# Kernel optimization log

Measured on AMD Instinct MI355X. Metric: run time of the kernel, lower is better.

Reference implementation:

```python
import jax, jax.numpy as jnp
import numpy as np

B, S = 4096, 4096
NS, FDIM = 16, 64


def _ln(x, g, b):
    mu = jnp.mean(x, axis=-1, keepdims=True)
    v = jnp.mean((x - mu) ** 2, axis=-1, keepdims=True)
    return (x - mu) / jnp.sqrt(v + 1e-5) * g + b


def _rolling_vol_mean(returns, w):
    # mean over all length-w windows of unbiased std (matches per-window torch.std loop)
    Bn, L = returns.shape
    z = jnp.zeros((Bn, 1), returns.dtype)
    c1 = jnp.concatenate([z, jnp.cumsum(returns, axis=1)], axis=1)
    c2 = jnp.concatenate([z, jnp.cumsum(returns * returns, axis=1)], axis=1)
    s = c1[:, w:] - c1[:, :-w]    # [B, L-w+1] window sums
    s2 = c2[:, w:] - c2[:, :-w]
    var = (s2 - s * s / w) / (w - 1)
    return jnp.mean(jnp.sqrt(jnp.maximum(var, 0.0)), axis=1, keepdims=True)


def setup_inputs() -> dict:
    key = jax.random.key(0)
    ks = jax.random.split(key, 24)
    r = lambda i, shp: jax.random.normal(ks[i], shp, jnp.float32) * 0.05
    return {
        'price_series': jax.random.uniform(ks[0], (B, S, 1), jnp.float32) * 10.0 + 1.0,
        're_W': r(1, (4, 4, 64)), 're_b': r(2, (4, 64)),
        're_g': jnp.ones((4, 64), jnp.float32), 're_beta': jnp.zeros((4, 64), jnp.float32),
        'rh_W1': r(3, (256, 64)), 'rh_b1': r(4, (64,)), 'rh_W2': r(5, (64, 4)), 'rh_b2': r(6, (4,)),
        'rv_W': r(7, (3, 128)), 'rv_b': r(8, (128,)),
        'rv_g': jnp.ones((128,), jnp.float32), 'rv_beta': jnp.zeros((128,), jnp.float32),
        'vs_W': r(9, (128, 128)), 'vs_b': r(10, (128,)),
        'vs_g': jnp.ones((128,), jnp.float32), 'vs_beta': jnp.zeros((128,), jnp.float32),
        'vc_W1': r(11, (256, 64)), 'vc_b1': r(12, (64,)), 'vc_W2': r(13, (64, 4)), 'vc_b2': r(14, (4,)),
        'emb': r(15, (NS, FDIM)),
        'cn_W1': r(16, (576, 128)), 'cn_b1': r(17, (128,)),
        'cn_W2': r(18, (128, 64)), 'cn_b2': r(19, (64,)),
        'cn_W3': r(20, (64, 1)), 'cn_b3': r(21, (1,)),
    }


def reference(price_series, re_W, re_b, re_g, re_beta, rh_W1, rh_b1, rh_W2, rh_b2,
              rv_W, rv_b, rv_g, rv_beta, vs_W, vs_b, vs_g, vs_beta,
              vc_W1, vc_b1, vc_W2, vc_b2, emb, cn_W1, cn_b1, cn_W2, cn_b2, cn_W3, cn_b3):
    prices = price_series[:, :, 0]            # [B,S]
    Bn, Sn = prices.shape
    # --- MarketRegimeEncoder: SMA-20 via prefix sums (the per-step torch loop) ---
    cs = jnp.cumsum(prices, axis=1)
    shifted = jnp.concatenate([jnp.zeros((Bn, 20), prices.dtype), cs[:, :-20]], axis=1)
    counts = jnp.minimum(jnp.arange(Sn) + 1, 20).astype(prices.dtype)
    sma20 = (cs - shifted) / counts           # (sma_5 is computed but unused in original)
    trend = jnp.mean((prices - sma20) / (sma20 + 1e-8), axis=1, keepdims=True)
    p10 = prices[:, Sn - 10:Sn - 9]
    momentum = (prices[:, -1:] - p10) / (p10 + 1e-8)
    pmean = jnp.mean(prices, axis=1, keepdims=True)
    mean_rev = (prices[:, -1:] - pmean) / (pmean + 1e-8)
    pstd = jnp.std(prices, axis=1, keepdims=True, ddof=1)
    cycle = pstd / (pmean + 1e-8)
    combined = jnp.concatenate([trend, momentum, mean_rev, cycle], axis=1)  # [B,4]
    h = jax.nn.relu(jnp.einsum('bi,kio->bko', combined, re_W) + re_b[None])  # [B,4,64]
    h = _ln(h, re_g[None], re_beta[None])
    regime_features = h.reshape(Bn, -1)        # [B,256] (trend|momentum|mean_rev|cycle)
    logits = jax.nn.relu(regime_features @ rh_W1 + rh_b1) @ rh_W2 + rh_b2
    regime_probs = jax.nn.softmax(logits, axis=1)
    # --- VolatilityEncodingModule ---
    logp = jnp.log(jnp.maximum(price_series, 1e-8))
    returns = jnp.diff(logp, axis=1)[:, :, 0]  # [B,S-1]
    vol_in = jnp.concatenate([_rolling_vol_mean(returns, w) for w in (5, 10, 20)], axis=1)  # [B,3]
    rv = _ln(jax.nn.relu(vol_in @ rv_W + rv_b), rv_g, rv_beta)
    vs = _ln(jax.nn.relu(rv @ vs_W + vs_b), vs_g, vs_beta)
    vol_features = jnp.concatenate([rv, vs], axis=1)  # [B,256]
    vlogits = jax.nn.relu(vol_features @ vc_W1 + vc_b1) @ vc_W2 + vc_b2
    vol_regime = jax.nn.softmax(vlogits, axis=1)
    # --- OptionsStrategyEncoder: vectorized over strategies ---
    mv = jnp.concatenate([regime_features, vol_features], axis=1)  # [B,512]
    mvp = mv @ cn_W1[:512]                    # [B,128]
    ep = emb @ cn_W1[512:]                    # [NS,128]
    h1 = jax.nn.relu(mvp[:, None, :] + ep[None, :, :] + cn_b1)  # [B,NS,128]
    h2 = jax.nn.relu(h1 @ cn_W2 + cn_b2)      # [B,NS,64]
    scores = (h2 @ cn_W3 + cn_b3)[:, :, 0]    # [B,NS]
    return regime_features, regime_probs, vol_features, vol_regime, scores
```

## Files before the change

kernel.cpp:

```cpp
#include <hip/hip_runtime.h>
#include <math.h>

#define NROWS 4096
#define SLEN  4096
#define RETN  4095
#define CHK   20

__global__ __launch_bounds__(256) void k_ep(const float* __restrict__ emb,
                                            const float* __restrict__ cn_W1,
                                            const float* __restrict__ cn_b1,
                                            float* __restrict__ ep) {
    int idx = blockIdx.x * 256 + threadIdx.x;
    if (idx >= 16 * 128) return;
    int n = idx >> 7, o = idx & 127;
    float acc = cn_b1[o];
    const float* w = cn_W1 + 512 * 128;
    for (int i = 0; i < 64; ++i) acc = fmaf(emb[n * 64 + i], w[i * 128 + o], acc);
    ep[idx] = acc;
}

__global__ void k_stats(const float* __restrict__ price,
                        float* __restrict__ combined,
                        float* __restrict__ volin) {
    __shared__ float scm[260 * CHK];
    __shared__ float red[6][4];

    const int tid = threadIdx.x;
    const int row = blockIdx.x;
    const float* pr = price + (size_t)row * SLEN;

    float pA = 0.f, pB = 0.f;
    if (tid == 0) { pA = pr[SLEN - 10]; pB = pr[SLEN - 1]; }

    if (tid < 40) { scm[tid] = 0.f; scm[258 * CHK + tid] = 0.f; }

    #pragma unroll
    for (int it = 0; it < 4; ++it) {
        const int i = it * 256 + tid;
        const float4 v = ((const float4*)pr)[i];
        *(float4*)&scm[(2 + (i >> 2)) * CHK + ((4 * i) & 15)] = v;
    }
    __syncthreads();

    const int s0 = tid * 16;

    float hb[20], x_[16];
    *(float4*)&hb[0] = *(const float4*)&scm[tid * CHK + 12];
    #pragma unroll
    for (int k = 0; k < 4; ++k)
        *(float4*)&hb[4 + 4 * k] = *(const float4*)&scm[(tid + 1) * CHK + 4 * k];
    #pragma unroll
    for (int k = 0; k < 4; ++k)
        *(float4*)&x_[4 * k] = *(const float4*)&scm[(tid + 2) * CHK + 4 * k];
    const float pn = scm[(tid + 3) * CHK];

    float W = 0.f;
    #pragma unroll
    for (int k = 0; k < 20; ++k) W += hb[k];
    float st = 0.f, s1p = 0.f, s2p = 0.f;
    #pragma unroll
    for (int d = 0; d < 16; ++d) {
        const float x = x_[d];
        W += x - hb[d];
        float inv_cnt = 0.05f;
        if (s0 == 0)                 inv_cnt = 1.0f / (float)(d + 1);
        else if (s0 == 16 && d < 3)  inv_cnt = 1.0f / (float)(17 + d);
        const float sma = W * inv_cnt;
        st  = fmaf(x - sma, __builtin_amdgcn_rcpf(sma + 1e-8f), st);
        s1p += x;
        s2p = fmaf(x, x, s2p);
    }

    float lg[17];
    #pragma unroll
    for (int d = 0; d < 16; ++d) lg[d] = __builtin_amdgcn_logf(fmaxf(x_[d], 1e-8f));
    lg[16] = __builtin_amdgcn_logf(fmaxf(pn, 1e-8f));
    float rs[36];
    #pragma unroll
    for (int d = 0; d < 16; ++d) rs[d] = lg[d + 1] - lg[d];

    __syncthreads();
    #pragma unroll
    for (int k = 0; k < 4; ++k)
        *(float4*)&scm[(tid + 2) * CHK + 4 * k] = *(const float4*)&rs[4 * k];
    __syncthreads();

    #pragma unroll
    for (int k = 0; k < 4; ++k)
        *(float4*)&rs[16 + 4 * k] = *(const float4*)&scm[(tid + 3) * CHK + 4 * k];
    *(float4*)&rs[32] = *(const float4*)&scm[(tid + 4) * CHK];

    float S5 = 0.f, Q5 = 0.f, S10 = 0.f, Q10 = 0.f, S20 = 0.f, Q20 = 0.f;
    #pragma unroll
    for (int j = 0; j < 20; ++j) {
        const float x = rs[j];
        S20 += x; Q20 = fmaf(x, x, Q20);
        if (j < 10) { S10 += x; Q10 = fmaf(x, x, Q10); }
        if (j < 5)  { S5  += x; Q5  = fmaf(x, x, Q5); }
    }

    #define SQT(S, Q, invw) \
        __builtin_amdgcn_sqrtf(fmaxf(fmaf(-(S) * (invw), (S), (Q)), 0.f))

    float v5 = 0.f, v10 = 0.f, v20 = 0.f;
    if (tid < 254) {
        #pragma unroll
        for (int d = 0; d < 16; ++d) {
            v5  += SQT(S5,  Q5,  0.2f);
            v10 += SQT(S10, Q10, 0.1f);
            v20 += SQT(S20, Q20, 0.05f);
            const float xo = rs[d], qo = xo * xo;
            const float a5 = rs[d + 5], a10 = rs[d + 10], a20 = rs[d + 20];
            S5  += a5  - xo;  Q5  = fmaf(a5,  a5,  Q5)  - qo;
            S10 += a10 - xo;  Q10 = fmaf(a10, a10, Q10) - qo;
            S20 += a20 - xo;  Q20 = fmaf(a20, a20, Q20) - qo;
        }
    } else {
        #pragma unroll
        for (int d = 0; d < 16; ++d) {
            const int i = s0 + d;
            if (i < 4091) v5  += SQT(S5,  Q5,  0.2f);
            if (i < 4086) v10 += SQT(S10, Q10, 0.1f);
            if (i < 4076) v20 += SQT(S20, Q20, 0.05f);
            const float xo = rs[d], qo = xo * xo;
            const float a5 = rs[d + 5], a10 = rs[d + 10], a20 = rs[d + 20];
            S5  += a5  - xo;  Q5  = fmaf(a5,  a5,  Q5)  - qo;
            S10 += a10 - xo;  Q10 = fmaf(a10, a10, Q10) - qo;
            S20 += a20 - xo;  Q20 = fmaf(a20, a20, Q20) - qo;
        }
    }
    #undef SQT

    {
        float vals[6] = {s1p, s2p, st, v5, v10, v20};
        const int lane = tid & 63, wid = tid >> 6;
        #pragma unroll
        for (int v = 0; v < 6; ++v) {
            float x = vals[v];
            for (int o = 32; o > 0; o >>= 1) x += __shfl_xor(x, o, 64);
            if (lane == 0) red[v][wid] = x;
        }
    }
    __syncthreads();
    if (tid == 0) {
        const float sum_p  = red[0][0] + red[0][1] + red[0][2] + red[0][3];
        const float sum_p2 = red[1][0] + red[1][1] + red[1][2] + red[1][3];
        const float sum_t  = red[2][0] + red[2][1] + red[2][2] + red[2][3];
        const float sv5    = red[3][0] + red[3][1] + red[3][2] + red[3][3];
        const float sv10   = red[4][0] + red[4][1] + red[4][2] + red[4][3];
        const float sv20   = red[5][0] + red[5][1] + red[5][2] + red[5][3];
        const float pmean = sum_p * (1.f / 4096.f);
        const float varp  = fmaf(-sum_p * (1.f / 4096.f), sum_p, sum_p2) * (1.f / 4095.f);
        const float pstd  = __builtin_amdgcn_sqrtf(fmaxf(varp, 0.f));
        const float ipm   = __builtin_amdgcn_rcpf(pmean + 1e-8f);
        combined[row * 4 + 0] = sum_t * (1.f / 4096.f);
        combined[row * 4 + 1] = (pB - pA) * __builtin_amdgcn_rcpf(pA + 1e-8f);
        combined[row * 4 + 2] = (pB - pmean) * ipm;
        combined[row * 4 + 3] = pstd * ipm;
        const float LN2 = 0.6931471805599453f;
        volin[row * 3 + 0] = sv5  * (LN2 * 0.5f                 / 4091.f);
        volin[row * 3 + 1] = sv10 * (LN2 * (1.f / 3.f)          / 4086.f);
        volin[row * 3 + 2] = sv20 * (LN2 * 0.22941573387056174f / 4076.f);
    }
}

__global__ __launch_bounds__(256) void k_mc(const float* __restrict__ combined,
                                            const float* __restrict__ volin,
                                            const float* __restrict__ re_W,  const float* __restrict__ re_b,
                                            const float* __restrict__ re_g,  const float* __restrict__ re_be,
                                            const float* __restrict__ rh_W1, const float* __restrict__ rh_b1,
                                            const float* __restrict__ rh_W2, const float* __restrict__ rh_b2,
                                            const float* __restrict__ rv_W,  const float* __restrict__ rv_b,
                                            const float* __restrict__ rv_g,  const float* __restrict__ rv_be,
                                            const float* __restrict__ vs_W,  const float* __restrict__ vs_b,
                                            const float* __restrict__ vs_g,  const float* __restrict__ vs_be,
                                            const float* __restrict__ vc_W1, const float* __restrict__ vc_b1,
                                            const float* __restrict__ vc_W2, const float* __restrict__ vc_b2,
                                            const float* __restrict__ cn_W1,
                                            const float* __restrict__ cn_W2,
                                            const float* __restrict__ cn_b2,
                                            const float* __restrict__ cn_W3,
                                            const float* __restrict__ cn_b3,
                                            const float* __restrict__ ep,
                                            float* __restrict__ out_rf, float* __restrict__ out_rp,
                                            float* __restrict__ out_vf, float* __restrict__ out_vr,
                                            float* __restrict__ scores) {
    __shared__ __align__(16) float w2s[128 * 64];
    __shared__ __align__(16) float epb[16][132];
    __shared__ __align__(16) float rf_lds[8][256];
    __shared__ __align__(16) float vf_lds[8][256];
    __shared__ __align__(16) float psx[4][8][128];
    __shared__ __align__(16) float mvp_s[8][132];
    __shared__ float hid_s[8][64];
    __shared__ float prt[4][8];
    __shared__ float cmb_s[8][4];
    __shared__ float vol_s[8][3];

    const int tid  = threadIdx.x;
    const int lane = tid & 63;
    const int wid  = tid >> 6;
    const int row0 = blockIdx.x * 8;

    #pragma unroll
    for (int k = 0; k < 8; ++k) {
        const int idx = k * 256 + tid;
        *(float4*)&w2s[4 * idx] = *(const float4*)(cn_W2 + 4 * idx);
    }
    {
        const int ns = tid >> 4, c8 = (tid & 15) * 8;
        *(float4*)&epb[ns][c8]     = *(const float4*)(ep + ns * 128 + c8);
        *(float4*)&epb[ns][c8 + 4] = *(const float4*)(ep + ns * 128 + c8 + 4);
    }
    if (tid < 32) cmb_s[tid >> 2][tid & 3] = combined[(size_t)(row0 + (tid >> 2)) * 4 + (tid & 3)];
    else if (tid < 56) { int t = tid - 32; vol_s[t / 3][t % 3] = volin[(size_t)(row0 + t / 3) * 3 + t % 3]; }
    __syncthreads();

    {
        const float* w = re_W + wid * 256;
        const float w0 = w[lane], w1 = w[64 + lane], w2 = w[128 + lane], w3 = w[192 + lane];
        const float b  = re_b[wid * 64 + lane];
        const float gg = re_g[wid * 64 + lane], bb = re_be[wid * 64 + lane];
        float h[8], sm[8], sq[8];
        #pragma unroll
        for (int r = 0; r < 8; ++r) {
            float v = fmaf(cmb_s[r][0], w0, fmaf(cmb_s[r][1], w1,
                      fmaf(cmb_s[r][2], w2, fmaf(cmb_s[r][3], w3, b))));
            h[r] = fmaxf(v, 0.f);
            sm[r] = h[r]; sq[r] = h[r] * h[r];
        }
        #pragma unroll
        for (int off = 32; off > 0; off >>= 1) {
            #pragma unroll
            for (int r = 0; r < 8; ++r) {
                sm[r] += __shfl_xor(sm[r], off, 64);
                sq[r] += __shfl_xor(sq[r], off, 64);
            }
        }
        #pragma unroll
        for (int r = 0; r < 8; ++r) {
            const float mu  = sm[r] * (1.f / 64.f);
            const float var = fmaxf(sq[r] * (1.f / 64.f) - mu * mu, 0.f);
            const float y = (h[r] - mu) * rsqrtf(var + 1e-5f) * gg + bb;
            rf_lds[r][wid * 64 + lane] = y;
            out_rf[(size_t)(row0 + r) * 256 + wid * 64 + lane] = y;
        }
    }
    __syncthreads();

    {
        const int i0 = wid * 64;
        float acc[8] = {0.f, 0.f, 0.f, 0.f, 0.f, 0.f, 0.f, 0.f};
        for (int i = 0; i < 64; ++i) {
            const float wv = rh_W1[(size_t)(i0 + i) * 64 + lane];
            #pragma unroll
            for (int r = 0; r < 8; ++r) acc[r] = fmaf(rf_lds[r][i0 + i], wv, acc[r]);
        }
        #pragma unroll
        for (int r = 0; r < 8; ++r) psx[wid][r][lane] = acc[r];
    }
    __syncthreads();

    for (int it = tid; it < 512; it += 256) {
        const int r = it >> 6, o = it & 63;
        const float v = psx[0][r][o] + psx[1][r][o] + psx[2][r][o] + psx[3][r][o] + rh_b1[o];
        hid_s[r][o] = fmaxf(v, 0.f);
    }
    __syncthreads();

    if (tid < 32) {
        const int r = tid >> 2, j = tid & 3;
        float acc = rh_b2[j];
        for (int i = 0; i < 64; ++i) acc = fmaf(hid_s[r][i], rh_W2[i * 4 + j], acc);
        float m = acc;
        m = fmaxf(m, __shfl_xor(m, 1, 64));
        m = fmaxf(m, __shfl_xor(m, 2, 64));
        const float e = expf(acc - m);
        float s = e;
        s += __shfl_xor(s, 1, 64);
        s += __shfl_xor(s, 2, 64);
        out_rp[(size_t)(row0 + r) * 4 + j] = e / s;
    }

    {
        const int o = tid & 127, g = tid >> 7, wv_ = tid >> 6;
        const float w0 = rv_W[o], w1 = rv_W[128 + o], w2 = rv_W[256 + o];
        const float b = rv_b[o], gg = rv_g[o], bb = rv_be[o];
        float h[4], sm[4], sq[4];
        #pragma unroll
        for (int r4 = 0; r4 < 4; ++r4) {
            const int r = g * 4 + r4;
            float v = fmaf(vol_s[r][0], w0, fmaf(vol_s[r][1], w1, fmaf(vol_s[r][2], w2, b)));
            h[r4] = fmaxf(v, 0.f);
            sm[r4] = h[r4]; sq[r4] = h[r4] * h[r4];
        }
        #pragma unroll
        for (int off = 32; off > 0; off >>= 1) {
            #pragma unroll
            for (int r4 = 0; r4 < 4; ++r4) {
                sm[r4] += __shfl_xor(sm[r4], off, 64);
                sq[r4] += __shfl_xor(sq[r4], off, 64);
            }
        }
        if (lane == 0) {
            #pragma unroll
            for (int r4 = 0; r4 < 4; ++r4) { prt[wv_][r4 * 2] = sm[r4]; prt[wv_][r4 * 2 + 1] = sq[r4]; }
        }
        __syncthreads();
        #pragma unroll
        for (int r4 = 0; r4 < 4; ++r4) {
            const float S = prt[2 * g][2 * r4]     + prt[2 * g + 1][2 * r4];
            const float Q = prt[2 * g][2 * r4 + 1] + prt[2 * g + 1][2 * r4 + 1];
            const float mu  = S * (1.f / 128.f);
            const float var = fmaxf(Q * (1.f / 128.f) - mu * mu, 0.f);
            const float y = (h[r4] - mu) * rsqrtf(var + 1e-5f) * gg + bb;
            vf_lds[g * 4 + r4][o] = y;
            out_vf[(size_t)(row0 + g * 4 + r4) * 256 + o] = y;
        }
    }
    __syncthreads();

    {
        const int o = tid & 127, g = tid >> 7, wv_ = tid >> 6;
        float acc[4];
        const float b = vs_b[o];
        #pragma unroll
        for (int r4 = 0; r4 < 4; ++r4) acc[r4] = b;
        for (int i = 0; i < 128; ++i) {
            const float wv = vs_W[(size_t)i * 128 + o];
            #pragma unroll
            for (int r4 = 0; r4 < 4; ++r4) acc[r4] = fmaf(vf_lds[g * 4 + r4][i], wv, acc[r4]);
        }
        const float gg = vs_g[o], bb = vs_be[o];
        float h[4], sm[4], sq[4];
        #pragma unroll
        for (int r4 = 0; r4 < 4; ++r4) {
            h[r4] = fmaxf(acc[r4], 0.f);
            sm[r4] = h[r4]; sq[r4] = h[r4] * h[r4];
        }
        #pragma unroll
        for (int off = 32; off > 0; off >>= 1) {
            #pragma unroll
            for (int r4 = 0; r4 < 4; ++r4) {
                sm[r4] += __shfl_xor(sm[r4], off, 64);
                sq[r4] += __shfl_xor(sq[r4], off, 64);
            }
        }
        __syncthreads();
        if (lane == 0) {
            #pragma unroll
            for (int r4 = 0; r4 < 4; ++r4) { prt[wv_][r4 * 2] = sm[r4]; prt[wv_][r4 * 2 + 1] = sq[r4]; }
        }
        __syncthreads();
        #pragma unroll
        for (int r4 = 0; r4 < 4; ++r4) {
            const float S = prt[2 * g][2 * r4]     + prt[2 * g + 1][2 * r4];
            const float Q = prt[2 * g][2 * r4 + 1] + prt[2 * g + 1][2 * r4 + 1];
            const float mu  = S * (1.f / 128.f);
            const float var = fmaxf(Q * (1.f / 128.f) - mu * mu, 0.f);
            const float y = (h[r4] - mu) * rsqrtf(var + 1e-5f) * gg + bb;
            vf_lds[g * 4 + r4][128 + o] = y;
            out_vf[(size_t)(row0 + g * 4 + r4) * 256 + 128 + o] = y;
        }
    }
    __syncthreads();

    {
        const int i0 = wid * 64;
        float acc[8] = {0.f, 0.f, 0.f, 0.f, 0.f, 0.f, 0.f, 0.f};
        for (int i = 0; i < 64; ++i) {
            const float wv = vc_W1[(size_t)(i0 + i) * 64 + lane];
            #pragma unroll
            for (int r = 0; r < 8; ++r) acc[r] = fmaf(vf_lds[r][i0 + i], wv, acc[r]);
        }
        #pragma unroll
        for (int r = 0; r < 8; ++r) psx[wid][r][lane] = acc[r];
    }
    __syncthreads();

    for (int it = tid; it < 512; it += 256) {
        const int r = it >> 6, o = it & 63;
        const float v = psx[0][r][o] + psx[1][r][o] + psx[2][r][o] + psx[3][r][o] + vc_b1[o];
        hid_s[r][o] = fmaxf(v, 0.f);
    }
    __syncthreads();
    if (tid < 32) {
        const int r = tid >> 2, j = tid & 3;
        float acc = vc_b2[j];
        for (int i = 0; i < 64; ++i) acc = fmaf(hid_s[r][i], vc_W2[i * 4 + j], acc);
        float m = acc;
        m = fmaxf(m, __shfl_xor(m, 1, 64));
        m = fmaxf(m, __shfl_xor(m, 2, 64));
        const float e = expf(acc - m);
        float s = e;
        s += __shfl_xor(s, 1, 64);
        s += __shfl_xor(s, 2, 64);
        out_vr[(size_t)(row0 + r) * 4 + j] = e / s;
    }
    __syncthreads();

    {
        const int p = lane >> 5;
        const int q = lane & 31;
        const float* mbase = (wid < 2) ? &rf_lds[0][0] + wid * 128
                                       : &vf_lds[0][0] + (wid - 2) * 128;
        float acc[8][4] = {{0.f}};
        #pragma unroll 8
        for (int s = 0; s < 64; ++s) {
            const int i = 2 * s + p;
            const float4 w1v = *(const float4*)(cn_W1 + (size_t)(wid * 128 + i) * 128 + 4 * q);
            #pragma unroll
            for (int r = 0; r < 8; ++r) {
                const float m = mbase[r * 256 + i];
                acc[r][0] = fmaf(m, w1v.x, acc[r][0]);
                acc[r][1] = fmaf(m, w1v.y, acc[r][1]);
                acc[r][2] = fmaf(m, w1v.z, acc[r][2]);
                acc[r][3] = fmaf(m, w1v.w, acc[r][3]);
            }
        }
        #pragma unroll
        for (int r = 0; r < 8; ++r) {
            #pragma unroll
            for (int k = 0; k < 4; ++k) acc[r][k] += __shfl_xor(acc[r][k], 32, 64);
        }
        if (p == 0) {
            #pragma unroll
            for (int r = 0; r < 8; ++r)
                *(float4*)&psx[wid][r][4 * q] =
                    make_float4(acc[r][0], acc[r][1], acc[r][2], acc[r][3]);
        }
    }
    __syncthreads();

    #pragma unroll
    for (int k = 0; k < 4; ++k) {
        const int idx = k * 256 + tid;
        const int r = idx >> 7, c = idx & 127;
        mvp_s[r][c] = psx[0][r][c] + psx[1][r][c] + psx[2][r][c] + psx[3][r][c];
    }
    __syncthreads();

    {
        const int ns = tid >> 4;
        const int t  = tid & 15;
        float acc[8][4];
        #pragma unroll
        for (int r = 0; r < 8; ++r)
            #pragma unroll
            for (int k = 0; k < 4; ++k) acc[r][k] = 0.f;

        #pragma unroll 2
        for (int c = 0; c < 128; c += 4) {
            float4 m4[8];
            #pragma unroll
            for (int r = 0; r < 8; ++r) m4[r] = *(const float4*)&mvp_s[r][c];
            const float4 e4 = *(const float4*)&epb[ns][c];
            {   const float4 w2v = *(const float4*)&w2s[(c + 0) * 64 + 4 * t];
                #pragma unroll
                for (int r = 0; r < 8; ++r) {
                    const float h = fmaxf(m4[r].x + e4.x, 0.f);
                    acc[r][0] = fmaf(h, w2v.x, acc[r][0]); acc[r][1] = fmaf(h, w2v.y, acc[r][1]);
                    acc[r][2] = fmaf(h, w2v.z, acc[r][2]); acc[r][3] = fmaf(h, w2v.w, acc[r][3]); } }
            {   const float4 w2v = *(const float4*)&w2s[(c + 1) * 64 + 4 * t];
                #pragma unroll
                for (int r = 0; r < 8; ++r) {
                    const float h = fmaxf(m4[r].y + e4.y, 0.f);
                    acc[r][0] = fmaf(h, w2v.x, acc[r][0]); acc[r][1] = fmaf(h, w2v.y, acc[r][1]);
                    acc[r][2] = fmaf(h, w2v.z, acc[r][2]); acc[r][3] = fmaf(h, w2v.w, acc[r][3]); } }
            {   const float4 w2v = *(const float4*)&w2s[(c + 2) * 64 + 4 * t];
                #pragma unroll
                for (int r = 0; r < 8; ++r) {
                    const float h = fmaxf(m4[r].z + e4.z, 0.f);
                    acc[r][0] = fmaf(h, w2v.x, acc[r][0]); acc[r][1] = fmaf(h, w2v.y, acc[r][1]);
                    acc[r][2] = fmaf(h, w2v.z, acc[r][2]); acc[r][3] = fmaf(h, w2v.w, acc[r][3]); } }
            {   const float4 w2v = *(const float4*)&w2s[(c + 3) * 64 + 4 * t];
                #pragma unroll
                for (int r = 0; r < 8; ++r) {
                    const float h = fmaxf(m4[r].w + e4.w, 0.f);
                    acc[r][0] = fmaf(h, w2v.x, acc[r][0]); acc[r][1] = fmaf(h, w2v.y, acc[r][1]);
                    acc[r][2] = fmaf(h, w2v.z, acc[r][2]); acc[r][3] = fmaf(h, w2v.w, acc[r][3]); } }
        }

        const float4 b2v = *(const float4*)(cn_b2 + 4 * t);
        const float4 w3v = *(const float4*)(cn_W3 + 4 * t);
        const float  b3v = cn_b3[0];
        #pragma unroll
        for (int r = 0; r < 8; ++r) {
            float s =      fmaxf(acc[r][0] + b2v.x, 0.f) * w3v.x;
            s = fmaf(fmaxf(acc[r][1] + b2v.y, 0.f), w3v.y, s);
            s = fmaf(fmaxf(acc[r][2] + b2v.z, 0.f), w3v.z, s);
            s = fmaf(fmaxf(acc[r][3] + b2v.w, 0.f), w3v.w, s);
            s += __shfl_xor(s, 1, 64);
            s += __shfl_xor(s, 2, 64);
            s += __shfl_xor(s, 4, 64);
            s += __shfl_xor(s, 8, 64);
            if (t == 0) scores[(size_t)(row0 + r) * 16 + ns] = s + b3v;
        }
    }
}

extern "C" void kernel_launch(void* const* d_in, const int* in_sizes, int n_in,
                              void* d_out, int out_size, void* d_ws, size_t ws_size,
                              hipStream_t stream) {
    (void)in_sizes; (void)n_in; (void)out_size; (void)ws_size;

    const float* price = (const float*)d_in[0];
    const float* re_W  = (const float*)d_in[1];
    const float* re_b  = (const float*)d_in[2];
    const float* re_g  = (const float*)d_in[3];
    const float* re_be = (const float*)d_in[4];
    const float* rh_W1 = (const float*)d_in[5];
    const float* rh_b1 = (const float*)d_in[6];
    const float* rh_W2 = (const float*)d_in[7];
    const float* rh_b2 = (const float*)d_in[8];
    const float* rv_W  = (const float*)d_in[9];
    const float* rv_b  = (const float*)d_in[10];
    const float* rv_g  = (const float*)d_in[11];
    const float* rv_be = (const float*)d_in[12];
    const float* vs_W  = (const float*)d_in[13];
    const float* vs_b  = (const float*)d_in[14];
    const float* vs_g  = (const float*)d_in[15];
    const float* vs_be = (const float*)d_in[16];
    const float* vc_W1 = (const float*)d_in[17];
    const float* vc_b1 = (const float*)d_in[18];
    const float* vc_W2 = (const float*)d_in[19];
    const float* vc_b2 = (const float*)d_in[20];
    const float* emb   = (const float*)d_in[21];
    const float* cn_W1 = (const float*)d_in[22];
    const float* cn_b1 = (const float*)d_in[23];
    const float* cn_W2 = (const float*)d_in[24];
    const float* cn_b2 = (const float*)d_in[25];
    const float* cn_W3 = (const float*)d_in[26];
    const float* cn_b3 = (const float*)d_in[27];

    float* out    = (float*)d_out;
    float* out_rf = out;
    float* out_rp = out_rf + 4096 * 256;
    float* out_vf = out_rp + 4096 * 4;
    float* out_vr = out_vf + 4096 * 256;
    float* out_sc = out_vr + 4096 * 4;

    float* ws       = (float*)d_ws;
    float* combined = ws;
    float* volin    = combined + 4096 * 4;
    float* ep       = volin + 4096 * 3;

    hipLaunchKernelGGL(k_ep,    dim3(8),    dim3(256), 0, stream, emb, cn_W1, cn_b1, ep);
    hipLaunchKernelGGL(k_stats, dim3(4096), dim3(256), 0, stream, price, combined, volin);
    hipLaunchKernelGGL(k_mc,    dim3(512),  dim3(256), 0, stream, combined, volin,
                       re_W, re_b, re_g, re_be, rh_W1, rh_b1, rh_W2, rh_b2,
                       rv_W, rv_b, rv_g, rv_be, vs_W, vs_b, vs_g, vs_be,
                       vc_W1, vc_b1, vc_W2, vc_b2,
                       cn_W1, cn_W2, cn_b2, cn_W3, cn_b3, ep,
                       out_rf, out_rp, out_vf, out_vr, out_sc);
}
```

Before: 97.76 us.

## Double k_mc block size to 512 threads, splitting rows across wave groups

The fused MLP kernel now launches 512 threads per block instead of 256, with the 8 rows per block split into two groups of 4 rows handled by separate wave sets. Each wave keeps fewer accumulators, so it needs fewer registers, and twice as many waves are available to hide latency across the 512 blocks. The cost is that weight loads from global memory (rh_W1, vc_W1, cn_W1, vs_W) are now issued twice per block, and there is more barrier overhead.

```diff
diff --git a/kernel.cpp b/kernel.cpp
--- a/kernel.cpp
+++ b/kernel.cpp
@@ -164,27 +164,27 @@
     }
 }
 
-__global__ __launch_bounds__(256) void k_mc(const float* __restrict__ combined,
-                                            const float* __restrict__ volin,
-                                            const float* __restrict__ re_W,  const float* __restrict__ re_b,
-                                            const float* __restrict__ re_g,  const float* __restrict__ re_be,
-                                            const float* __restrict__ rh_W1, const float* __restrict__ rh_b1,
-                                            const float* __restrict__ rh_W2, const float* __restrict__ rh_b2,
-                                            const float* __restrict__ rv_W,  const float* __restrict__ rv_b,
-                                            const float* __restrict__ rv_g,  const float* __restrict__ rv_be,
-                                            const float* __restrict__ vs_W,  const float* __restrict__ vs_b,
-                                            const float* __restrict__ vs_g,  const float* __restrict__ vs_be,
-                                            const float* __restrict__ vc_W1, const float* __restrict__ vc_b1,
-                                            const float* __restrict__ vc_W2, const float* __restrict__ vc_b2,
-                                            const float* __restrict__ cn_W1,
-                                            const float* __restrict__ cn_W2,
-                                            const float* __restrict__ cn_b2,
-                                            const float* __restrict__ cn_W3,
-                                            const float* __restrict__ cn_b3,
-                                            const float* __restrict__ ep,
-                                            float* __restrict__ out_rf, float* __restrict__ out_rp,
-                                            float* __restrict__ out_vf, float* __restrict__ out_vr,
-                                            float* __restrict__ scores) {
+__global__ __launch_bounds__(512, 4) void k_mc(const float* __restrict__ combined,
+                                               const float* __restrict__ volin,
+                                               const float* __restrict__ re_W,  const float* __restrict__ re_b,
+                                               const float* __restrict__ re_g,  const float* __restrict__ re_be,
+                                               const float* __restrict__ rh_W1, const float* __restrict__ rh_b1,
+                                               const float* __restrict__ rh_W2, const float* __restrict__ rh_b2,
+                                               const float* __restrict__ rv_W,  const float* __restrict__ rv_b,
+                                               const float* __restrict__ rv_g,  const float* __restrict__ rv_be,
+                                               const float* __restrict__ vs_W,  const float* __restrict__ vs_b,
+                                               const float* __restrict__ vs_g,  const float* __restrict__ vs_be,
+                                               const float* __restrict__ vc_W1, const float* __restrict__ vc_b1,
+                                               const float* __restrict__ vc_W2, const float* __restrict__ vc_b2,
+                                               const float* __restrict__ cn_W1,
+                                               const float* __restrict__ cn_W2,
+                                               const float* __restrict__ cn_b2,
+                                               const float* __restrict__ cn_W3,
+                                               const float* __restrict__ cn_b3,
+                                               const float* __restrict__ ep,
+                                               float* __restrict__ out_rf, float* __restrict__ out_rp,
+                                               float* __restrict__ out_vf, float* __restrict__ out_vr,
+                                               float* __restrict__ scores) {
     __shared__ __align__(16) float w2s[128 * 64];
     __shared__ __align__(16) float epb[16][132];
     __shared__ __align__(16) float rf_lds[8][256];
@@ -192,7 +192,7 @@
     __shared__ __align__(16) float psx[4][8][128];
     __shared__ __align__(16) float mvp_s[8][132];
     __shared__ float hid_s[8][64];
-    __shared__ float prt[4][8];
+    __shared__ float prt[8][4];
     __shared__ float cmb_s[8][4];
     __shared__ float vol_s[8][3];
 
@@ -202,66 +202,69 @@
     const int row0 = blockIdx.x * 8;
 
     #pragma unroll
-    for (int k = 0; k < 8; ++k) {
-        const int idx = k * 256 + tid;
+    for (int k = 0; k < 4; ++k) {
+        const int idx = k * 512 + tid;
         *(float4*)&w2s[4 * idx] = *(const float4*)(cn_W2 + 4 * idx);
     }
     {
-        const int ns = tid >> 4, c8 = (tid & 15) * 8;
-        *(float4*)&epb[ns][c8]     = *(const float4*)(ep + ns * 128 + c8);
-        *(float4*)&epb[ns][c8 + 4] = *(const float4*)(ep + ns * 128 + c8 + 4);
+        const int ns = tid >> 5, c4 = (tid & 31) * 4;
+        *(float4*)&epb[ns][c4] = *(const float4*)(ep + ns * 128 + c4);
     }
     if (tid < 32) cmb_s[tid >> 2][tid & 3] = combined[(size_t)(row0 + (tid >> 2)) * 4 + (tid & 3)];
     else if (tid < 56) { int t = tid - 32; vol_s[t / 3][t % 3] = volin[(size_t)(row0 + t / 3) * 3 + t % 3]; }
     __syncthreads();
 
-    {
-        const float* w = re_W + wid * 256;
+    const int role = wid & 3;
+    const int rg   = (wid >> 2) * 4;
+
+    {
+        const float* w = re_W + role * 256;
         const float w0 = w[lane], w1 = w[64 + lane], w2 = w[128 + lane], w3 = w[192 + lane];
-        const float b  = re_b[wid * 64 + lane];
-        const float gg = re_g[wid * 64 + lane], bb = re_be[wid * 64 + lane];
-        float h[8], sm[8], sq[8];
-        #pragma unroll
-        for (int r = 0; r < 8; ++r) {
-            float v = fmaf(cmb_s[r][0], w0, fmaf(cmb_s[r][1], w1,
-                      fmaf(cmb_s[r][2], w2, fmaf(cmb_s[r][3], w3, b))));
+        const float b  = re_b[role * 64 + lane];
+        const float gg = re_g[role * 64 + lane], bb = re_be[role * 64 + lane];
+        float h[4], sm[4], sq[4];
+        #pragma unroll
+        for (int r = 0; r < 4; ++r) {
+            const int rr = rg + r;
+            float v = fmaf(cmb_s[rr][0], w0, fmaf(cmb_s[rr][1], w1,
+                      fmaf(cmb_s[rr][2], w2, fmaf(cmb_s[rr][3], w3, b))));
             h[r] = fmaxf(v, 0.f);
             sm[r] = h[r]; sq[r] = h[r] * h[r];
         }
         #pragma unroll
         for (int off = 32; off > 0; off >>= 1) {
             #pragma unroll
-            for (int r = 0; r < 8; ++r) {
+            for (int r = 0; r < 4; ++r) {
                 sm[r] += __shfl_xor(sm[r], off, 64);
                 sq[r] += __shfl_xor(sq[r], off, 64);
             }
         }
         #pragma unroll
-        for (int r = 0; r < 8; ++r) {
+        for (int r = 0; r < 4; ++r) {
             const float mu  = sm[r] * (1.f / 64.f);
             const float var = fmaxf(sq[r] * (1.f / 64.f) - mu * mu, 0.f);
             const float y = (h[r] - mu) * rsqrtf(var + 1e-5f) * gg + bb;
-            rf_lds[r][wid * 64 + lane] = y;
-            out_rf[(size_t)(row0 + r) * 256 + wid * 64 + lane] = y;
-        }
-    }
-    __syncthreads();
-
-    {
-        const int i0 = wid * 64;
-        float acc[8] = {0.f, 0.f, 0.f, 0.f, 0.f, 0.f, 0.f, 0.f};
+            rf_lds[rg + r][role * 64 + lane] = y;
+            out_rf[(size_t)(row0 + rg + r) * 256 + role * 64 + lane] = y;
+        }
+    }
+    __syncthreads();
+
+    {
+        const int i0 = role * 64;
+        float acc[4] = {0.f, 0.f, 0.f, 0.f};
         for (int i = 0; i < 64; ++i) {
             const float wv = rh_W1[(size_t)(i0 + i) * 64 + lane];
             #pragma unroll
-            for (int r = 0; r < 8; ++r) acc[r] = fmaf(rf_lds[r][i0 + i], wv, acc[r]);
-        }
-        #pragma unroll
-        for (int r = 0; r < 8; ++r) psx[wid][r][lane] = acc[r];
-    }
-    __syncthreads();
-
-    for (int it = tid; it < 512; it += 256) {
-        const int r = it >> 6, o = it & 63;
+            for (int r = 0; r < 4; ++r) acc[r] = fmaf(rf_lds[rg + r][i0 + i], wv, acc[r]);
+        }
+        #pragma unroll
+        for (int r = 0; r < 4; ++r) psx[role][rg + r][lane] = acc[r];
+    }
+    __syncthreads();
+
+    {
+        const int r = tid >> 6, o = tid & 63;
         const float v = psx[0][r][o] + psx[1][r][o] + psx[2][r][o] + psx[3][r][o] + rh_b1[o];
         hid_s[r][o] = fmaxf(v, 0.f);
     }
@@ -282,103 +285,102 @@
     }
 
     {
-        const int o = tid & 127, g = tid >> 7, wv_ = tid >> 6;
+        const int o = tid & 127, g = tid >> 7;
         const float w0 = rv_W[o], w1 = rv_W[128 + o], w2 = rv_W[256 + o];
         const float b = rv_b[o], gg = rv_g[o], bb = rv_be[o];
-        float h[4], sm[4], sq[4];
-        #pragma unroll
-        for (int r4 = 0; r4 < 4; ++r4) {
-            const int r = g * 4 + r4;
+        float h[2], sm[2], sq[2];
+        #pragma unroll
+        for (int r2 = 0; r2 < 2; ++r2) {
+            const int r = g * 2 + r2;
             float v = fmaf(vol_s[r][0], w0, fmaf(vol_s[r][1], w1, fmaf(vol_s[r][2], w2, b)));
-            h[r4] = fmaxf(v, 0.f);
-            sm[r4] = h[r4]; sq[r4] = h[r4] * h[r4];
+            h[r2] = fmaxf(v, 0.f);
+            sm[r2] = h[r2]; sq[r2] = h[r2] * h[r2];
         }
         #pragma unroll
         for (int off = 32; off > 0; off >>= 1) {
             #pragma unroll
-            for (int r4 = 0; r4 < 4; ++r4) {
-                sm[r4] += __shfl_xor(sm[r4], off, 64);
-                sq[r4] += __shfl_xor(sq[r4], off, 64);
+            for (int r2 = 0; r2 < 2; ++r2) {
+                sm[r2] += __shfl_xor(sm[r2], off, 64);
+                sq[r2] += __shfl_xor(sq[r2], off, 64);
             }
         }
         if (lane == 0) {
             #pragma unroll
-            for (int r4 = 0; r4 < 4; ++r4) { prt[wv_][r4 * 2] = sm[r4]; prt[wv_][r4 * 2 + 1] = sq[r4]; }
+            for (int r2 = 0; r2 < 2; ++r2) { prt[wid][r2 * 2] = sm[r2]; prt[wid][r2 * 2 + 1] = sq[r2]; }
         }
         __syncthreads();
         #pragma unroll
-        for (int r4 = 0; r4 < 4; ++r4) {
-            const float S = prt[2 * g][2 * r4]     + prt[2 * g + 1][2 * r4];
-            const float Q = prt[2 * g][2 * r4 + 1] + prt[2 * g + 1][2 * r4 + 1];
+        for (int r2 = 0; r2 < 2; ++r2) {
+            const float S = prt[2 * g][2 * r2]     + prt[2 * g + 1][2 * r2];
+            const float Q = prt[2 * g][2 * r2 + 1] + prt[2 * g + 1][2 * r2 + 1];
             const float mu  = S * (1.f / 128.f);
             const float var = fmaxf(Q * (1.f / 128.f) - mu * mu, 0.f);
-            const float y = (h[r4] - mu) * rsqrtf(var + 1e-5f) * gg + bb;
-            vf_lds[g * 4 + r4][o] = y;
-            out_vf[(size_t)(row0 + g * 4 + r4) * 256 + o] = y;
-        }
-    }
-    __syncthreads();
-
-    {
-        const int o = tid & 127, g = tid >> 7, wv_ = tid >> 6;
-        float acc[4];
+            const float y = (h[r2] - mu) * rsqrtf(var + 1e-5f) * gg + bb;
+            vf_lds[g * 2 + r2][o] = y;
+            out_vf[(size_t)(row0 + g * 2 + r2) * 256 + o] = y;
+        }
+    }
+    __syncthreads();
+
+    {
+        const int o = tid & 127, g = tid >> 7;
+        float acc[2];
         const float b = vs_b[o];
-        #pragma unroll
-        for (int r4 = 0; r4 < 4; ++r4) acc[r4] = b;
+        acc[0] = b; acc[1] = b;
         for (int i = 0; i < 128; ++i) {
             const float wv = vs_W[(size_t)i * 128 + o];
             #pragma unroll
-            for (int r4 = 0; r4 < 4; ++r4) acc[r4] = fmaf(vf_lds[g * 4 + r4][i], wv, acc[r4]);
+            for (int r2 = 0; r2 < 2; ++r2) acc[r2] = fmaf(vf_lds[g * 2 + r2][i], wv, acc[r2]);
         }
         const float gg = vs_g[o], bb = vs_be[o];
-        float h[4], sm[4], sq[4];
-        #pragma unroll
-        for (int r4 = 0; r4 < 4; ++r4) {
-            h[r4] = fmaxf(acc[r4], 0.f);
-            sm[r4] = h[r4]; sq[r4] = h[r4] * h[r4];
+        float h[2], sm[2], sq[2];
+        #pragma unroll
+        for (int r2 = 0; r2 < 2; ++r2) {
+            h[r2] = fmaxf(acc[r2], 0.f);
+            sm[r2] = h[r2]; sq[r2] = h[r2] * h[r2];
         }
         #pragma unroll
         for (int off = 32; off > 0; off >>= 1) {
             #pragma unroll
-            for (int r4 = 0; r4 < 4; ++r4) {
-                sm[r4] += __shfl_xor(sm[r4], off, 64);
-                sq[r4] += __shfl_xor(sq[r4], off, 64);
+            for (int r2 = 0; r2 < 2; ++r2) {
+                sm[r2] += __shfl_xor(sm[r2], off, 64);
+                sq[r2] += __shfl_xor(sq[r2], off, 64);
             }
         }
         __syncthreads();
         if (lane == 0) {
             #pragma unroll
-            for (int r4 = 0; r4 < 4; ++r4) { prt[wv_][r4 * 2] = sm[r4]; prt[wv_][r4 * 2 + 1] = sq[r4]; }
+            for (int r2 = 0; r2 < 2; ++r2) { prt[wid][r2 * 2] = sm[r2]; prt[wid][r2 * 2 + 1] = sq[r2]; }
         }
         __syncthreads();
         #pragma unroll
-        for (int r4 = 0; r4 < 4; ++r4) {
-            const float S = prt[2 * g][2 * r4]     + prt[2 * g + 1][2 * r4];
-            const float Q = prt[2 * g][2 * r4 + 1] + prt[2 * g + 1][2 * r4 + 1];
+        for (int r2 = 0; r2 < 2; ++r2) {
+            const float S = prt[2 * g][2 * r2]     + prt[2 * g + 1][2 * r2];
+            const float Q = prt[2 * g][2 * r2 + 1] + prt[2 * g + 1][2 * r2 + 1];
             const float mu  = S * (1.f / 128.f);
             const float var = fmaxf(Q * (1.f / 128.f) - mu * mu, 0.f);
-            const float y = (h[r4] - mu) * rsqrtf(var + 1e-5f) * gg + bb;
-            vf_lds[g * 4 + r4][128 + o] = y;
-            out_vf[(size_t)(row0 + g * 4 + r4) * 256 + 128 + o] = y;
-        }
-    }
-    __syncthreads();
-
-    {
-        const int i0 = wid * 64;
-        float acc[8] = {0.f, 0.f, 0.f, 0.f, 0.f, 0.f, 0.f, 0.f};
+            const float y = (h[r2] - mu) * rsqrtf(var + 1e-5f) * gg + bb;
+            vf_lds[g * 2 + r2][128 + o] = y;
+            out_vf[(size_t)(row0 + g * 2 + r2) * 256 + 128 + o] = y;
+        }
+    }
+    __syncthreads();
+
+    {
+        const int i0 = role * 64;
+        float acc[4] = {0.f, 0.f, 0.f, 0.f};
         for (int i = 0; i < 64; ++i) {
             const float wv = vc_W1[(size_t)(i0 + i) * 64 + lane];
             #pragma unroll
-            for (int r = 0; r < 8; ++r) acc[r] = fmaf(vf_lds[r][i0 + i], wv, acc[r]);
-        }
-        #pragma unroll
-        for (int r = 0; r < 8; ++r) psx[wid][r][lane] = acc[r];
-    }
-    __syncthreads();
-
-    for (int it = tid; it < 512; it += 256) {
-        const int r = it >> 6, o = it & 63;
+            for (int r = 0; r < 4; ++r) acc[r] = fmaf(vf_lds[rg + r][i0 + i], wv, acc[r]);
+        }
+        #pragma unroll
+        for (int r = 0; r < 4; ++r) psx[role][rg + r][lane] = acc[r];
+    }
+    __syncthreads();
+
+    {
+        const int r = tid >> 6, o = tid & 63;
         const float v = psx[0][r][o] + psx[1][r][o] + psx[2][r][o] + psx[3][r][o] + vc_b1[o];
         hid_s[r][o] = fmaxf(v, 0.f);
     }
@@ -401,16 +403,16 @@
     {
         const int p = lane >> 5;
         const int q = lane & 31;
-        const float* mbase = (wid < 2) ? &rf_lds[0][0] + wid * 128
-                                       : &vf_lds[0][0] + (wid - 2) * 128;
-        float acc[8][4] = {{0.f}};
+        const float* mbase = (role < 2) ? &rf_lds[0][0] + role * 128
+                                        : &vf_lds[0][0] + (role - 2) * 128;
+        float acc[4][4] = {{0.f}};
         #pragma unroll 8
         for (int s = 0; s < 64; ++s) {
             const int i = 2 * s + p;
-            const float4 w1v = *(const float4*)(cn_W1 + (size_t)(wid * 128 + i) * 128 + 4 * q);
-            #pragma unroll
-            for (int r = 0; r < 8; ++r) {
-                const float m = mbase[r * 256 + i];
+            const float4 w1v = *(const float4*)(cn_W1 + (size_t)(role * 128 + i) * 128 + 4 * q);
+            #pragma unroll
+            for (int r = 0; r < 4; ++r) {
+                const float m = mbase[(rg + r) * 256 + i];
                 acc[r][0] = fmaf(m, w1v.x, acc[r][0]);
                 acc[r][1] = fmaf(m, w1v.y, acc[r][1]);
                 acc[r][2] = fmaf(m, w1v.z, acc[r][2]);
@@ -418,63 +420,65 @@
             }
         }
         #pragma unroll
-        for (int r = 0; r < 8; ++r) {
+        for (int r = 0; r < 4; ++r) {
             #pragma unroll
             for (int k = 0; k < 4; ++k) acc[r][k] += __shfl_xor(acc[r][k], 32, 64);
         }
         if (p == 0) {
             #pragma unroll
-            for (int r = 0; r < 8; ++r)
-                *(float4*)&psx[wid][r][4 * q] =
+            for (int r = 0; r < 4; ++r)
+                *(float4*)&psx[role][rg + r][4 * q] =
                     make_float4(acc[r][0], acc[r][1], acc[r][2], acc[r][3]);
         }
     }
     __syncthreads();
 
     #pragma unroll
-    for (int k = 0; k < 4; ++k) {
-        const int idx = k * 256 + tid;
+    for (int k = 0; k < 2; ++k) {
+        const int idx = k * 512 + tid;
         const int r = idx >> 7, c = idx & 127;
         mvp_s[r][c] = psx[0][r][c] + psx[1][r][c] + psx[2][r][c] + psx[3][r][c];
     }
     __syncthreads();
 
     {
-        const int ns = tid >> 4;
-        const int t  = tid & 15;
-        float acc[8][4];
-        #pragma unroll
-        for (int r = 0; r < 8; ++r)
+        const int rgB = tid >> 8;
+        const int nst = tid & 255;
+        const int ns  = nst >> 4;
+        const int t   = nst & 15;
+        float acc[4][4];
+        #pragma unroll
+        for (int r = 0; r < 4; ++r)
             #pragma unroll
             for (int k = 0; k < 4; ++k) acc[r][k] = 0.f;
 
         #pragma unroll 2
         for (int c = 0; c < 128; c += 4) {
-            float4 m4[8];
-            #pragma unroll
-            for (int r = 0; r < 8; ++r) m4[r] = *(const float4*)&mvp_s[r][c];
+            float4 m4[4];
+            #pragma unroll
+            for (int r = 0; r < 4; ++r) m4[r] = *(const float4*)&mvp_s[rgB * 4 + r][c];
             const float4 e4 = *(const float4*)&epb[ns][c];
             {   const float4 w2v = *(const float4*)&w2s[(c + 0) * 64 + 4 * t];
                 #pragma unroll
-                for (int r = 0; r < 8; ++r) {
+                for (int r = 0; r < 4; ++r) {
                     const float h = fmaxf(m4[r].x + e4.x, 0.f);
                     acc[r][0] = fmaf(h, w2v.x, acc[r][0]); acc[r][1] = fmaf(h, w2v.y, acc[r][1]);
                     acc[r][2] = fmaf(h, w2v.z, acc[r][2]); acc[r][3] = fmaf(h, w2v.w, acc[r][3]); } }
             {   const float4 w2v = *(const float4*)&w2s[(c + 1) * 64 + 4 * t];
                 #pragma unroll
-                for (int r = 0; r < 8; ++r) {
+                for (int r = 0; r < 4; ++r) {
                     const float h = fmaxf(m4[r].y + e4.y, 0.f);
                     acc[r][0] = fmaf(h, w2v.x, acc[r][0]); acc[r][1] = fmaf(h, w2v.y, acc[r][1]);
                     acc[r][2] = fmaf(h, w2v.z, acc[r][2]); acc[r][3] = fmaf(h, w2v.w, acc[r][3]); } }
             {   const float4 w2v = *(const float4*)&w2s[(c + 2) * 64 + 4 * t];
                 #pragma unroll
-                for (int r = 0; r < 8; ++r) {
+                for (int r = 0; r < 4; ++r) {
                     const float h = fmaxf(m4[r].z + e4.z, 0.f);
                     acc[r][0] = fmaf(h, w2v.x, acc[r][0]); acc[r][1] = fmaf(h, w2v.y, acc[r][1]);
                     acc[r][2] = fmaf(h, w2v.z, acc[r][2]); acc[r][3] = fmaf(h, w2v.w, acc[r][3]); } }
             {   const float4 w2v = *(const float4*)&w2s[(c + 3) * 64 + 4 * t];
                 #pragma unroll
-                for (int r = 0; r < 8; ++r) {
+                for (int r = 0; r < 4; ++r) {
                     const float h = fmaxf(m4[r].w + e4.w, 0.f);
                     acc[r][0] = fmaf(h, w2v.x, acc[r][0]); acc[r][1] = fmaf(h, w2v.y, acc[r][1]);
                     acc[r][2] = fmaf(h, w2v.z, acc[r][2]); acc[r][3] = fmaf(h, w2v.w, acc[r][3]); } }
@@ -484,7 +488,7 @@
         const float4 w3v = *(const float4*)(cn_W3 + 4 * t);
         const float  b3v = cn_b3[0];
         #pragma unroll
-        for (int r = 0; r < 8; ++r) {
+        for (int r = 0; r < 4; ++r) {
             float s =      fmaxf(acc[r][0] + b2v.x, 0.f) * w3v.x;
             s = fmaf(fmaxf(acc[r][1] + b2v.y, 0.f), w3v.y, s);
             s = fmaf(fmaxf(acc[r][2] + b2v.z, 0.f), w3v.z, s);
@@ -493,7 +497,7 @@
             s += __shfl_xor(s, 2, 64);
             s += __shfl_xor(s, 4, 64);
             s += __shfl_xor(s, 8, 64);
-            if (t == 0) scores[(size_t)(row0 + r) * 16 + ns] = s + b3v;
+            if (t == 0) scores[(size_t)(row0 + rgB * 4 + r) * 16 + ns] = s + b3v;
         }
     }
 }
@@ -546,7 +550,7 @@
 
     hipLaunchKernelGGL(k_ep,    dim3(8),    dim3(256), 0, stream, emb, cn_W1, cn_b1, ep);
     hipLaunchKernelGGL(k_stats, dim3(4096), dim3(256), 0, stream, price, combined, volin);
-    hipLaunchKernelGGL(k_mc,    dim3(512),  dim3(256), 0, stream, combined, volin,
+    hipLaunchKernelGGL(k_mc,    dim3(512),  dim3(512), 0, stream, combined, volin,
                        re_W, re_b, re_g, re_be, rh_W1, rh_b1, rh_W2, rh_b2,
                        rv_W, rv_b, rv_g, rv_be, vs_W, vs_b, vs_g, vs_be,
                        vc_W1, vc_b1, vc_W2, vc_b2,
```

Measured after the change: 122.1 us. 1.25x slower.
